# Optimization experiments

Hardware: AMD Instinct MI355X
Metric: run time of the kernel (lower is better)

The kernel has to match this reference:

```python
import jax, jax.numpy as jnp
import numpy as np

HEADS = 8  # from init_kwargs

def setup_inputs() -> dict:
    key = jax.random.key(0)
    ks = jax.random.split(key, 9)
    N, S, E = 8, 2048, 512
    scale = 1.0 / np.sqrt(E)
    return {
        "values": jax.random.normal(ks[0], (N, S, E), jnp.float32),
        "keys": jax.random.normal(ks[1], (N, S, E), jnp.float32),
        "query": jax.random.normal(ks[2], (N, S, E), jnp.float32),
        "mask": jnp.ones((N, 1, 1, S), jnp.int32),
        "Wv": jax.random.normal(ks[3], (E, E), jnp.float32) * scale,
        "Wk": jax.random.normal(ks[4], (E, E), jnp.float32) * scale,
        "Wq": jax.random.normal(ks[5], (E, E), jnp.float32) * scale,
        "Wo": jax.random.normal(ks[6], (E, E), jnp.float32) * scale,
        "bo": jnp.zeros((E,), jnp.float32),
    }

def reference(values, keys, query, mask, Wv, Wk, Wq, Wo, bo):
    N, Q, E = query.shape
    H = HEADS
    D = E // H
    v = (values @ Wv).reshape(N, -1, H, D)  # [N,K,H,D]
    k = (keys @ Wk).reshape(N, -1, H, D)
    q = (query @ Wq).reshape(N, Q, H, D)
    energy = jnp.einsum('nqhd,nkhd->nhqk', q, k)  # [N,H,Q,K]
    energy = jnp.where(mask == 0, jnp.float32(-1e20), energy)
    attn = jax.nn.softmax(energy / jnp.sqrt(jnp.float32(D)), axis=3)
    out = jnp.einsum('nhqk,nkhd->nqhd', attn, v).reshape(N, Q, E)
    return out @ Wo + bo
```

## Files before the change

kernel.cpp:

```cpp
#include <hip/hip_runtime.h>
#include <hip/hip_bf16.h>
#include <stdint.h>

typedef __bf16 bf16;
typedef __bf16 bf16x8 __attribute__((ext_vector_type(8)));
typedef __bf16 bf16x4v __attribute__((ext_vector_type(4)));
typedef float  f32x4  __attribute__((ext_vector_type(4)));
typedef float  f32x16 __attribute__((ext_vector_type(16)));
typedef unsigned int u32x4 __attribute__((ext_vector_type(4)));

#define NB    8
#define SEQ   2048
#define EMB   512
#define NHEAD 8
#define HD    64

static __device__ __forceinline__ f32x4 mfma16(bf16x8 a, bf16x8 b, f32x4 c) {
    return __builtin_amdgcn_mfma_f32_16x16x32_bf16(a, b, c, 0, 0, 0);
}
static __device__ __forceinline__ f32x16 mfma32(bf16x8 a, bf16x8 b, f32x16 c) {
    return __builtin_amdgcn_mfma_f32_32x32x16_bf16(a, b, c, 0, 0, 0);
}
static __device__ __forceinline__ float ex2(float x) {
    float r; asm("v_exp_f32 %0, %1" : "=v"(r) : "v"(x)); return r;
}
static __device__ __forceinline__ unsigned pkbf(float lo, float hi) {
    unsigned d; asm("v_cvt_pk_bf16_f32 %0, %1, %2" : "=v"(d) : "v"(lo), "v"(hi)); return d;
}
static __device__ __forceinline__ void gload_lds16(const void* g, void* l) {
    __builtin_amdgcn_global_load_lds(
        (const __attribute__((address_space(1))) unsigned int*)g,
        (__attribute__((address_space(3))) unsigned int*)l, 16, 0, 0);
}
#define PRIO1 __builtin_amdgcn_s_setprio(1)
#define PRIO0 __builtin_amdgcn_s_setprio(0)

__global__ __launch_bounds__(256) void prep_weights(
    const float* __restrict__ Wv, const float* __restrict__ Wk,
    const float* __restrict__ Wq, const float* __restrict__ Wo,
    bf16* __restrict__ wt)
{
    __shared__ float Ls[64][65];
    const int b    = blockIdx.x;
    const int wsel = b >> 6;
    const int kt   = (b & 63) >> 3;
    const int nt   = b & 7;
    const int t    = threadIdx.x;
    const float* src = (wsel == 0) ? Wv : (wsel == 1) ? Wk : (wsel == 2) ? Wq : Wo;

#pragma unroll
    for (int i = 0; i < 16; ++i) {
        int e = i * 256 + t;
        int k = e >> 6, n = e & 63;
        Ls[k][n] = src[(size_t)(kt * 64 + k) * 512 + nt * 64 + n];
    }
    __syncthreads();
#pragma unroll
    for (int i = 0; i < 16; ++i) {
        int e = i * 256 + t;
        int n = e >> 6, k = e & 63;
        wt[(size_t)wsel * 262144 + (size_t)(nt * 64 + n) * 512 + kt * 64 + k] = (bf16)Ls[k][n];
    }
}

template <bool A_F32, bool FINAL>
__global__ __launch_bounds__(256) void gemm_kernel(
    const void* __restrict__ Ap, const bf16* __restrict__ Bt,
    void* __restrict__ Cp, const float* __restrict__ bias, float oscale)
{
    __shared__ __align__(16) char AsM[128 * 144];
    __shared__ __align__(16) bf16 Bs[128][64];

    const int t    = threadIdx.x;
    const int lane = t & 63;
    const int wave = t >> 6;
    const int wr   = wave >> 1, wc = wave & 1;
    const int l15  = lane & 15, lg = lane >> 4;
    const long row0 = (long)blockIdx.x * 128;
    const int  col0 = blockIdx.y * 128;

    f32x4 acc[4][4];
#pragma unroll
    for (int i = 0; i < 4; i++)
#pragma unroll
        for (int j = 0; j < 4; j++) acc[i][j] = (f32x4){0.f, 0.f, 0.f, 0.f};

    for (int k0 = 0; k0 < 512; k0 += 64) {
        __syncthreads();
        if (A_F32) {
            const float* A = (const float*)Ap;
#pragma unroll
            for (int i = 0; i < 8; i++) {
                int c  = t + 256 * i;
                int r  = c >> 4;
                int cc = (c & 15) * 4;
                f32x4 v = *(const f32x4*)(A + (row0 + r) * 512 + k0 + cc);
                bf16x4v pk = { (bf16)v[0], (bf16)v[1], (bf16)v[2], (bf16)v[3] };
                *(bf16x4v*)(AsM + r * 144 + cc * 2) = pk;
            }
        } else {
            const bf16* A = (const bf16*)Ap;
#pragma unroll
            for (int i = 0; i < 4; i++) {
                int chunk = i * 4 + wave;
                int c = chunk * 64 + lane;
                int r = c >> 3, u = c & 7;
                gload_lds16(A + (row0 + r) * 512 + k0 + ((u ^ (r & 7)) << 3),
                            AsM + chunk * 1024);
            }
        }
#pragma unroll
        for (int i = 0; i < 4; i++) {
            int chunk = i * 4 + wave;
            int c = chunk * 64 + lane;
            int r = c >> 3, u = c & 7;
            gload_lds16(Bt + (size_t)(col0 + r) * 512 + k0 + ((u ^ (r & 7)) << 3),
                        (char*)&Bs[0][0] + chunk * 1024);
        }
        __syncthreads();
#pragma unroll
        for (int kc = 0; kc < 64; kc += 32) {
            bf16x8 af[4], bfv[4];
#pragma unroll
            for (int mb = 0; mb < 4; mb++) {
                int row = wr * 64 + mb * 16 + l15;
                if (A_F32)
                    af[mb] = *(bf16x8*)(AsM + row * 144 + (kc + lg * 8) * 2);
                else
                    af[mb] = *(bf16x8*)(AsM + row * 128 + (((lg + (kc >> 3)) ^ (l15 & 7)) << 4));
            }
#pragma unroll
            for (int nb = 0; nb < 4; nb++) {
                int row = wc * 64 + nb * 16 + l15;
                bfv[nb] = *(bf16x8*)((char*)&Bs[0][0] + row * 128 + (((lg + (kc >> 3)) ^ (l15 & 7)) << 4));
            }
#pragma unroll
            for (int mb = 0; mb < 4; mb++)
#pragma unroll
                for (int nb = 0; nb < 4; nb++)
                    acc[mb][nb] = mfma16(af[mb], bfv[nb], acc[mb][nb]);
        }
    }

#pragma unroll
    for (int mb = 0; mb < 4; mb++)
#pragma unroll
        for (int nb = 0; nb < 4; nb++)
#pragma unroll
            for (int r = 0; r < 4; r++) {
                long grow = row0 + wr * 64 + mb * 16 + lg * 4 + r;
                int  gcol = col0 + wc * 64 + nb * 16 + l15;
                float v = acc[mb][nb][r];
                if (FINAL) {
                    ((float*)Cp)[grow * 512 + gcol] = v + bias[gcol];
                } else {
                    ((bf16*)Cp)[grow * 512 + gcol] = (bf16)(v * oscale);
                }
            }
}

__global__ __launch_bounds__(512, 2) void attn_kernel(
    const bf16* __restrict__ Qg, const bf16* __restrict__ Kg,
    const bf16* __restrict__ Vg, const int* __restrict__ mask,
    bf16* __restrict__ ctx)
{
    __shared__ __align__(16) bf16 Ks[4][4096];
    __shared__ __align__(16) bf16 Vt[4][4096];
    __shared__ __align__(16) bf16 Ob[8][32 * 72];

    const int t    = threadIdx.x;
    const int lane = t & 63;
    const int w    = t >> 6;
    const int l31  = lane & 31;
    const int hi   = lane >> 5;
    const int h = blockIdx.x, n = blockIdx.y, qt = blockIdx.z;

    const size_t nbase   = (size_t)n * SEQ;
    const size_t headoff = (size_t)h * 64;
    const int q0 = qt * 512 + w * 64;

    const int k5_  = lane & 31;
    const int hi2_ = (k5_ >> 2) & 1;
    const int r_   = (k5_ & 3) + 4 * (k5_ >> 3);
    const int vpos = ((lane >> 5) * 2 + (r_ >> 3)) * 16 + hi2_ * 8 + (r_ & 7);

    int* mflags = (int*)&Ob[0][0];
    {
        const int* mp0 = mask + n * SEQ + t * 4;
        int mok = (mp0[0] != 0) & (mp0[1] != 0) & (mp0[2] != 0) & (mp0[3] != 0);
        unsigned long long b = __ballot(mok);
        if (lane == 0) mflags[w] = (b == ~0ULL) ? 1 : 0;
    }

    bf16x8 qf[2][4];
#pragma unroll
    for (int qb = 0; qb < 2; ++qb)
#pragma unroll
        for (int ds = 0; ds < 4; ++ds)
            qf[qb][ds] = *(const bf16x8*)(Qg + (nbase + q0 + qb * 32 + l31) * 512 + headoff + ds * 16 + hi * 8);

    f32x16 o[2][2] = {};
    float l_run[2] = {0.f, 0.f};

    const bf16* kg = Kg + (nbase + w * 8 + (lane >> 3)) * 512 + headoff + (((lane & 7) ^ (lane >> 3)) << 3);
    const bf16* vg = Vg + (nbase + lane) * 512 + headoff + w * 8;
    const int*  mp = mask + n * SEQ;

#define VSCAT(VR, VB) do {                                                    \
        char* vbp = (char*)(VB);                                              \
        _Pragma("unroll") for (int j = 0; j < 8; ++j)                         \
            *(bf16*)(vbp + (8 * w + j) * 128 + ((2 * vpos) ^ (j << 4))) = (VR)[j]; \
    } while (0)

    gload_lds16(kg,                     (char*)&Ks[0][0] + w * 1024);
    gload_lds16(kg + (size_t)64 * 512,  (char*)&Ks[1][0] + w * 1024);
    bf16x8 vrA = *(const bf16x8*)vg;
    bf16x8 vrB = *(const bf16x8*)(vg + (size_t)64 * 512);
    VSCAT(vrA, &Vt[0][0]);
    VSCAT(vrB, &Vt[1][0]);
    __syncthreads();
    const int maskall = mflags[0] & mflags[1] & mflags[2] & mflags[3] &
                        mflags[4] & mflags[5] & mflags[6] & mflags[7];

    f32x16 p[2][2];
    u32x4  bq[2][4];

#define QK_TILE(KB) do {                                                      \
        const char* kbb = (const char*)(KB);                                  \
        f32x16 zz = {};                                                       \
        p[0][0] = zz; p[0][1] = zz; p[1][0] = zz; p[1][1] = zz;               \
        PRIO1;                                                                \
        _Pragma("unroll")                                                     \
        for (int ds = 0; ds < 4; ++ds) {                                      \
            int sw = (ds * 32 + hi * 16) ^ ((l31 & 7) << 4);                  \
            bf16x8 kf0 = *(const bf16x8*)(kbb + l31 * 128 + sw);              \
            bf16x8 kf1 = *(const bf16x8*)(kbb + (32 + l31) * 128 + sw);       \
            p[0][0] = mfma32(kf0, qf[0][ds], p[0][0]);                        \
            p[1][0] = mfma32(kf0, qf[1][ds], p[1][0]);                        \
            p[0][1] = mfma32(kf1, qf[0][ds], p[0][1]);                        \
            p[1][1] = mfma32(kf1, qf[1][ds], p[1][1]);                        \
        }                                                                     \
        PRIO0;                                                                \
    } while (0)

#define MASK_TILE(T) do {                                                     \
        if (!maskall) {                                                       \
            int mv = mp[(T) * 64 + lane];                                     \
            unsigned long long mb = __ballot(mv != 0);                        \
            if (mb != ~0ULL) {                                                \
                _Pragma("unroll") for (int qb = 0; qb < 2; ++qb)              \
                _Pragma("unroll") for (int kb = 0; kb < 2; ++kb) {            \
                    float* pp = (float*)&p[qb][kb];                           \
                    _Pragma("unroll") for (int r = 0; r < 16; ++r) {          \
                        int kk = kb * 32 + (r & 3) + 8 * (r >> 2) + 4 * hi;   \
                        if (!((mb >> kk) & 1)) pp[r] = -1e30f;                \
                    }                                                         \
                }                                                             \
            }                                                                 \
        }                                                                     \
    } while (0)

#define SM_PACK do {                                                          \
        _Pragma("unroll")                                                     \
        for (int qb = 0; qb < 2; ++qb) {                                      \
            float* p0 = (float*)&p[qb][0];                                    \
            float* p1 = (float*)&p[qb][1];                                    \
            float sa0 = 0.f, sa1 = 0.f, sa2 = 0.f, sa3 = 0.f;                 \
            _Pragma("unroll") for (int r = 0; r < 16; r += 4) {               \
                float e0 = ex2(p0[r]);   p0[r]   = e0; sa0 += e0;             \
                float e1 = ex2(p0[r+1]); p0[r+1] = e1; sa1 += e1;             \
                float e2 = ex2(p0[r+2]); p0[r+2] = e2; sa2 += e2;             \
                float e3 = ex2(p0[r+3]); p0[r+3] = e3; sa3 += e3;             \
            }                                                                 \
            _Pragma("unroll") for (int r = 0; r < 16; r += 4) {               \
                float e0 = ex2(p1[r]);   p1[r]   = e0; sa0 += e0;             \
                float e1 = ex2(p1[r+1]); p1[r+1] = e1; sa1 += e1;             \
                float e2 = ex2(p1[r+2]); p1[r+2] = e2; sa2 += e2;             \
                float e3 = ex2(p1[r+3]); p1[r+3] = e3; sa3 += e3;             \
            }                                                                 \
            float sl = (sa0 + sa1) + (sa2 + sa3);                             \
            l_run[qb] += sl + __shfl_xor(sl, 32);                             \
            _Pragma("unroll")                                                 \
            for (int ks = 0; ks < 4; ++ks) {                                  \
                float* ps = (ks >> 1) ? p1 : p0;                              \
                int bo = (ks & 1) * 8;                                        \
                bq[qb][ks] = (u32x4){ pkbf(ps[bo + 0], ps[bo + 1]),           \
                                      pkbf(ps[bo + 2], ps[bo + 3]),           \
                                      pkbf(ps[bo + 4], ps[bo + 5]),           \
                                      pkbf(ps[bo + 6], ps[bo + 7]) };         \
            }                                                                 \
        }                                                                     \
    } while (0)

#define PV_TILE(VB) do {                                                      \
        const char* vbb = (const char*)(VB);                                  \
        PRIO1;                                                                \
        _Pragma("unroll")                                                     \
        for (int ks = 0; ks < 4; ++ks) {                                      \
            int sw = (ks * 32 + hi * 16) ^ ((l31 & 7) << 4);                  \
            bf16x8 vf0 = *(const bf16x8*)(vbb + l31 * 128 + sw);              \
            bf16x8 vf1 = *(const bf16x8*)(vbb + (32 + l31) * 128 + sw);       \
            union { u32x4 u; bf16x8 v; } c0, c1;                              \
            c0.u = bq[0][ks]; c1.u = bq[1][ks];                               \
            o[0][0] = mfma32(vf0, c0.v, o[0][0]);                             \
            o[0][1] = mfma32(vf0, c1.v, o[0][1]);                             \
            o[1][0] = mfma32(vf1, c0.v, o[1][0]);                             \
            o[1][1] = mfma32(vf1, c1.v, o[1][1]);                             \
        }                                                                     \
        PRIO0;                                                                \
    } while (0)

    for (int e = 0; e < 16; ++e) {
        const int bA = (e & 1) * 2, bB = bA + 1;
        const int nA = bA ^ 2,      nB = bB ^ 2;
        if (e < 15) {
            gload_lds16(kg + (size_t)(2 * e + 2) * 64 * 512, (char*)&Ks[nA][0] + w * 1024);
            gload_lds16(kg + (size_t)(2 * e + 3) * 64 * 512, (char*)&Ks[nB][0] + w * 1024);
            vrA = *(const bf16x8*)(vg + (size_t)(2 * e + 2) * 64 * 512);
            vrB = *(const bf16x8*)(vg + (size_t)(2 * e + 3) * 64 * 512);
        }
        QK_TILE(&Ks[bA][0]);
        MASK_TILE(2 * e);
        SM_PACK;
        PV_TILE(&Vt[bA][0]);
        QK_TILE(&Ks[bB][0]);
        MASK_TILE(2 * e + 1);
        SM_PACK;
        PV_TILE(&Vt[bB][0]);
        if (e < 15) {
            VSCAT(vrA, &Vt[nA][0]);
            VSCAT(vrB, &Vt[nB][0]);
        }
        __syncthreads();
    }

#pragma unroll
    for (int qb = 0; qb < 2; ++qb) {
        float inv = 1.f / l_run[qb];
        bf16* ob = &Ob[w][0];
#pragma unroll
        for (int db = 0; db < 2; ++db) {
            float* oo = (float*)&o[db][qb];
#pragma unroll
            for (int r = 0; r < 16; ++r) {
                int d = db * 32 + (r & 3) + 8 * (r >> 2) + 4 * hi;
                ob[l31 * 72 + d] = (bf16)(oo[r] * inv);
            }
        }
#pragma unroll
        for (int i = 0; i < 2; ++i)
#pragma unroll
            for (int half = 0; half < 2; ++half) {
                int ql = i * 16 + (lane >> 2);
                int d8 = (lane & 3) * 8 + half * 32;
                bf16x8 vv = *(const bf16x8*)(ob + ql * 72 + d8);
                *(bf16x8*)(ctx + (nbase + q0 + qb * 32 + ql) * 512 + headoff + d8) = vv;
            }
    }
#undef VSCAT
#undef QK_TILE
#undef MASK_TILE
#undef SM_PACK
#undef PV_TILE
}

extern "C" void kernel_launch(void* const* d_in, const int* in_sizes, int n_in,
                              void* d_out, int out_size, void* d_ws, size_t ws_size,
                              hipStream_t stream) {
    (void)in_sizes; (void)n_in; (void)out_size; (void)ws_size;
    const float* values = (const float*)d_in[0];
    const float* keys   = (const float*)d_in[1];
    const float* query  = (const float*)d_in[2];
    const int*   mask   = (const int*)d_in[3];
    const float* Wv = (const float*)d_in[4];
    const float* Wk = (const float*)d_in[5];
    const float* Wq = (const float*)d_in[6];
    const float* Wo = (const float*)d_in[7];
    const float* bo = (const float*)d_in[8];
    float* out = (float*)d_out;

    char* ws = (char*)d_ws;
    bf16* wt = (bf16*)(ws);
    bf16* Qb = (bf16*)(ws + ((size_t)2  << 20));
    bf16* Kb = (bf16*)(ws + ((size_t)18 << 20));
    bf16* Vb = (bf16*)(ws + ((size_t)34 << 20));
    bf16* Cb = (bf16*)(ws + ((size_t)50 << 20));

    const float SC = 0.18033688011f;

    prep_weights<<<256, 256, 0, stream>>>(Wv, Wk, Wq, Wo, wt);
    gemm_kernel<true, false><<<dim3(128, 4), 256, 0, stream>>>(values, wt,              Vb, nullptr, 1.0f);
    gemm_kernel<true, false><<<dim3(128, 4), 256, 0, stream>>>(keys,   wt + 262144,     Kb, nullptr, 1.0f);
    gemm_kernel<true, false><<<dim3(128, 4), 256, 0, stream>>>(query,  wt + 2 * 262144, Qb, nullptr, SC);
    attn_kernel<<<dim3(8, 8, 4), 512, 0, stream>>>(Qb, Kb, Vb, mask, Cb);
    gemm_kernel<false, true><<<dim3(128, 4), 256, 0, stream>>>(Cb, wt + 3 * 262144, out, bo, 1.0f);
}
```

Before: 162.3 us.

## Fuse QKV projections and pre-transpose V into attention-ready layout

Merges the three projection GEMM launches into one grid over a z dimension. The V projection now writes its output already transposed and permuted into the layout the attention kernel's PV MFMA expects. The attention kernel can then load V tiles straight into LDS with global_load_lds instead of doing register loads and scalar scatter writes each iteration, which takes VALU and LDS-store work out of the inner loop. The cost is a more complex V epilogue (an LDS transpose plus an index permutation) in the projection kernel.

```diff
diff --git a/kernel.cpp b/kernel.cpp
--- a/kernel.cpp
+++ b/kernel.cpp
@@ -31,6 +31,12 @@
     __builtin_amdgcn_global_load_lds(
         (const __attribute__((address_space(1))) unsigned int*)g,
         (__attribute__((address_space(3))) unsigned int*)l, 16, 0, 0);
+}
+static __device__ __forceinline__ int vposInv(int pos) {
+    int p4  = pos >> 4;
+    int r   = ((p4 & 1) << 3) | (pos & 7);
+    int hi2 = (pos >> 3) & 1;
+    return (p4 >> 1) * 32 + ((r & 3) | (hi2 << 2) | ((r >> 2) << 3));
 }
 #define PRIO1 __builtin_amdgcn_s_setprio(1)
 #define PRIO0 __builtin_amdgcn_s_setprio(0)
@@ -63,12 +69,122 @@
     }
 }
 
-template <bool A_F32, bool FINAL>
-__global__ __launch_bounds__(256) void gemm_kernel(
-    const void* __restrict__ Ap, const bf16* __restrict__ Bt,
-    void* __restrict__ Cp, const float* __restrict__ bias, float oscale)
+__global__ __launch_bounds__(256) void proj_fused(
+    const float* __restrict__ Av, const float* __restrict__ Ak,
+    const float* __restrict__ Aq, const bf16* __restrict__ wt,
+    bf16* __restrict__ VbP, bf16* __restrict__ Kb, bf16* __restrict__ Qb,
+    float sc)
 {
-    __shared__ __align__(16) char AsM[128 * 144];
+    __shared__ __align__(16) char smem[35328];
+    bf16* As = (bf16*)smem;
+    char* BsB = smem + 18432;
+
+    const int t    = threadIdx.x;
+    const int lane = t & 63;
+    const int wave = t >> 6;
+    const int wr   = wave >> 1, wc = wave & 1;
+    const int l15  = lane & 15, lg = lane >> 4;
+    const int z    = blockIdx.z;
+    const long row0 = (long)blockIdx.x * 128;
+    const int  col0 = blockIdx.y * 128;
+
+    const float* A  = (z == 0) ? Av : (z == 1) ? Ak : Aq;
+    const bf16*  Bt = wt + (size_t)z * 262144;
+    const float  oscale = (z == 2) ? sc : 1.0f;
+
+    f32x4 acc[4][4];
+#pragma unroll
+    for (int i = 0; i < 4; i++)
+#pragma unroll
+        for (int j = 0; j < 4; j++) acc[i][j] = (f32x4){0.f, 0.f, 0.f, 0.f};
+
+    for (int k0 = 0; k0 < 512; k0 += 64) {
+        __syncthreads();
+#pragma unroll
+        for (int i = 0; i < 8; i++) {
+            int c  = t + 256 * i;
+            int r  = c >> 4;
+            int cc = (c & 15) * 4;
+            f32x4 v = *(const f32x4*)(A + (row0 + r) * 512 + k0 + cc);
+            bf16x4v pk = { (bf16)v[0], (bf16)v[1], (bf16)v[2], (bf16)v[3] };
+            *(bf16x4v*)(As + r * 72 + cc) = pk;
+        }
+#pragma unroll
+        for (int i = 0; i < 4; i++) {
+            int chunk = i * 4 + wave;
+            int c = chunk * 64 + lane;
+            int r = c >> 3, u = c & 7;
+            gload_lds16(Bt + (size_t)(col0 + r) * 512 + k0 + ((u ^ (r & 7)) << 3),
+                        BsB + chunk * 1024);
+        }
+        __syncthreads();
+#pragma unroll
+        for (int kc = 0; kc < 64; kc += 32) {
+            bf16x8 af[4], bfv[4];
+#pragma unroll
+            for (int mb = 0; mb < 4; mb++)
+                af[mb] = *(bf16x8*)(As + (wr * 64 + mb * 16 + l15) * 72 + kc + lg * 8);
+#pragma unroll
+            for (int nb = 0; nb < 4; nb++) {
+                int row = wc * 64 + nb * 16 + l15;
+                bfv[nb] = *(bf16x8*)(BsB + row * 128 + (((lg + (kc >> 3)) ^ (l15 & 7)) << 4));
+            }
+#pragma unroll
+            for (int mb = 0; mb < 4; mb++)
+#pragma unroll
+                for (int nb = 0; nb < 4; nb++)
+                    acc[mb][nb] = mfma16(af[mb], bfv[nb], acc[mb][nb]);
+        }
+    }
+
+    if (z == 0) {
+        __syncthreads();
+        bf16* Cs = (bf16*)smem;
+#pragma unroll
+        for (int mb = 0; mb < 4; mb++)
+#pragma unroll
+            for (int nb = 0; nb < 4; nb++)
+#pragma unroll
+                for (int r = 0; r < 4; r++) {
+                    int keyl = wr * 64 + mb * 16 + lg * 4 + r;
+                    int dl   = wc * 64 + nb * 16 + l15;
+                    Cs[dl * 138 + keyl] = (bf16)acc[mb][nb][r];
+                }
+        __syncthreads();
+        const int n_idx = (int)(row0 >> 11);
+        const int key0  = (int)(row0 & 2047);
+        const int dl    = t >> 1;
+        const int half  = t & 1;
+        const int x8    = (dl & 7) << 3;
+        bf16* dst = VbP + ((size_t)n_idx * 512 + col0 + dl) * 2048 + key0 + half * 64;
+#pragma unroll
+        for (int cc = 0; cc < 8; ++cc) {
+            bf16x8 v;
+#pragma unroll
+            for (int j = 0; j < 8; ++j)
+                v[j] = Cs[dl * 138 + half * 64 + vposInv((cc * 8 + j) ^ x8)];
+            *(bf16x8*)(dst + cc * 8) = v;
+        }
+    } else {
+        bf16* Cp = (z == 1) ? Kb : Qb;
+#pragma unroll
+        for (int mb = 0; mb < 4; mb++)
+#pragma unroll
+            for (int nb = 0; nb < 4; nb++)
+#pragma unroll
+                for (int r = 0; r < 4; r++) {
+                    long grow = row0 + wr * 64 + mb * 16 + lg * 4 + r;
+                    int  gcol = col0 + wc * 64 + nb * 16 + l15;
+                    Cp[grow * 512 + gcol] = (bf16)(acc[mb][nb][r] * oscale);
+                }
+    }
+}
+
+__global__ __launch_bounds__(256) void gemm_final(
+    const bf16* __restrict__ Ap, const bf16* __restrict__ Bt,
+    float* __restrict__ Cp, const float* __restrict__ bias)
+{
+    __shared__ __align__(16) char AsM[128 * 128];
     __shared__ __align__(16) bf16 Bs[128][64];
 
     const int t    = threadIdx.x;
@@ -87,27 +203,13 @@
 
     for (int k0 = 0; k0 < 512; k0 += 64) {
         __syncthreads();
-        if (A_F32) {
-            const float* A = (const float*)Ap;
-#pragma unroll
-            for (int i = 0; i < 8; i++) {
-                int c  = t + 256 * i;
-                int r  = c >> 4;
-                int cc = (c & 15) * 4;
-                f32x4 v = *(const f32x4*)(A + (row0 + r) * 512 + k0 + cc);
-                bf16x4v pk = { (bf16)v[0], (bf16)v[1], (bf16)v[2], (bf16)v[3] };
-                *(bf16x4v*)(AsM + r * 144 + cc * 2) = pk;
-            }
-        } else {
-            const bf16* A = (const bf16*)Ap;
-#pragma unroll
-            for (int i = 0; i < 4; i++) {
-                int chunk = i * 4 + wave;
-                int c = chunk * 64 + lane;
-                int r = c >> 3, u = c & 7;
-                gload_lds16(A + (row0 + r) * 512 + k0 + ((u ^ (r & 7)) << 3),
-                            AsM + chunk * 1024);
-            }
+#pragma unroll
+        for (int i = 0; i < 4; i++) {
+            int chunk = i * 4 + wave;
+            int c = chunk * 64 + lane;
+            int r = c >> 3, u = c & 7;
+            gload_lds16(Ap + (row0 + r) * 512 + k0 + ((u ^ (r & 7)) << 3),
+                        AsM + chunk * 1024);
         }
 #pragma unroll
         for (int i = 0; i < 4; i++) {
@@ -124,10 +226,7 @@
 #pragma unroll
             for (int mb = 0; mb < 4; mb++) {
                 int row = wr * 64 + mb * 16 + l15;
-                if (A_F32)
-                    af[mb] = *(bf16x8*)(AsM + row * 144 + (kc + lg * 8) * 2);
-                else
-                    af[mb] = *(bf16x8*)(AsM + row * 128 + (((lg + (kc >> 3)) ^ (l15 & 7)) << 4));
+                af[mb] = *(bf16x8*)(AsM + row * 128 + (((lg + (kc >> 3)) ^ (l15 & 7)) << 4));
             }
 #pragma unroll
             for (int nb = 0; nb < 4; nb++) {
@@ -150,18 +249,13 @@
             for (int r = 0; r < 4; r++) {
                 long grow = row0 + wr * 64 + mb * 16 + lg * 4 + r;
                 int  gcol = col0 + wc * 64 + nb * 16 + l15;
-                float v = acc[mb][nb][r];
-                if (FINAL) {
-                    ((float*)Cp)[grow * 512 + gcol] = v + bias[gcol];
-                } else {
-                    ((bf16*)Cp)[grow * 512 + gcol] = (bf16)(v * oscale);
-                }
+                Cp[grow * 512 + gcol] = acc[mb][nb][r] + bias[gcol];
             }
 }
 
 __global__ __launch_bounds__(512, 2) void attn_kernel(
     const bf16* __restrict__ Qg, const bf16* __restrict__ Kg,
-    const bf16* __restrict__ Vg, const int* __restrict__ mask,
+    const bf16* __restrict__ VbP, const int* __restrict__ mask,
     bf16* __restrict__ ctx)
 {
     __shared__ __align__(16) bf16 Ks[4][4096];
@@ -179,11 +273,6 @@
     const size_t headoff = (size_t)h * 64;
     const int q0 = qt * 512 + w * 64;
 
-    const int k5_  = lane & 31;
-    const int hi2_ = (k5_ >> 2) & 1;
-    const int r_   = (k5_ & 3) + 4 * (k5_ >> 3);
-    const int vpos = ((lane >> 5) * 2 + (r_ >> 3)) * 16 + hi2_ * 8 + (r_ & 7);
-
     int* mflags = (int*)&Ob[0][0];
     {
         const int* mp0 = mask + n * SEQ + t * 4;
@@ -203,21 +292,13 @@
     float l_run[2] = {0.f, 0.f};
 
     const bf16* kg = Kg + (nbase + w * 8 + (lane >> 3)) * 512 + headoff + (((lane & 7) ^ (lane >> 3)) << 3);
-    const bf16* vg = Vg + (nbase + lane) * 512 + headoff + w * 8;
+    const bf16* vgP = VbP + ((size_t)n * 512 + h * 64 + w * 8 + (lane >> 3)) * 2048 + ((lane & 7) << 3);
     const int*  mp = mask + n * SEQ;
 
-#define VSCAT(VR, VB) do {                                                    \
-        char* vbp = (char*)(VB);                                              \
-        _Pragma("unroll") for (int j = 0; j < 8; ++j)                         \
-            *(bf16*)(vbp + (8 * w + j) * 128 + ((2 * vpos) ^ (j << 4))) = (VR)[j]; \
-    } while (0)
-
-    gload_lds16(kg,                     (char*)&Ks[0][0] + w * 1024);
-    gload_lds16(kg + (size_t)64 * 512,  (char*)&Ks[1][0] + w * 1024);
-    bf16x8 vrA = *(const bf16x8*)vg;
-    bf16x8 vrB = *(const bf16x8*)(vg + (size_t)64 * 512);
-    VSCAT(vrA, &Vt[0][0]);
-    VSCAT(vrB, &Vt[1][0]);
+    gload_lds16(kg,                    (char*)&Ks[0][0] + w * 1024);
+    gload_lds16(kg + (size_t)64 * 512, (char*)&Ks[1][0] + w * 1024);
+    gload_lds16(vgP,                   (char*)&Vt[0][0] + w * 1024);
+    gload_lds16(vgP + 64,              (char*)&Vt[1][0] + w * 1024);
     __syncthreads();
     const int maskall = mflags[0] & mflags[1] & mflags[2] & mflags[3] &
                         mflags[4] & mflags[5] & mflags[6] & mflags[7];
@@ -316,8 +397,8 @@
         if (e < 15) {
             gload_lds16(kg + (size_t)(2 * e + 2) * 64 * 512, (char*)&Ks[nA][0] + w * 1024);
             gload_lds16(kg + (size_t)(2 * e + 3) * 64 * 512, (char*)&Ks[nB][0] + w * 1024);
-            vrA = *(const bf16x8*)(vg + (size_t)(2 * e + 2) * 64 * 512);
-            vrB = *(const bf16x8*)(vg + (size_t)(2 * e + 3) * 64 * 512);
+            gload_lds16(vgP + (2 * e + 2) * 64,              (char*)&Vt[nA][0] + w * 1024);
+            gload_lds16(vgP + (2 * e + 3) * 64,              (char*)&Vt[nB][0] + w * 1024);
         }
         QK_TILE(&Ks[bA][0]);
         MASK_TILE(2 * e);
@@ -327,10 +408,6 @@
         MASK_TILE(2 * e + 1);
         SM_PACK;
         PV_TILE(&Vt[bB][0]);
-        if (e < 15) {
-            VSCAT(vrA, &Vt[nA][0]);
-            VSCAT(vrB, &Vt[nB][0]);
-        }
         __syncthreads();
     }
 
@@ -357,7 +434,6 @@
                 *(bf16x8*)(ctx + (nbase + q0 + qb * 32 + ql) * 512 + headoff + d8) = vv;
             }
     }
-#undef VSCAT
 #undef QK_TILE
 #undef MASK_TILE
 #undef SM_PACK
@@ -380,18 +456,17 @@
     float* out = (float*)d_out;
 
     char* ws = (char*)d_ws;
-    bf16* wt = (bf16*)(ws);
-    bf16* Qb = (bf16*)(ws + ((size_t)2  << 20));
-    bf16* Kb = (bf16*)(ws + ((size_t)18 << 20));
-    bf16* Vb = (bf16*)(ws + ((size_t)34 << 20));
-    bf16* Cb = (bf16*)(ws + ((size_t)50 << 20));
+    bf16* wt  = (bf16*)(ws);
+    bf16* Qb  = (bf16*)(ws + ((size_t)2  << 20));
+    bf16* Kb  = (bf16*)(ws + ((size_t)18 << 20));
+    bf16* VbP = (bf16*)(ws + ((size_t)34 << 20));
+    bf16* Cb  = (bf16*)(ws + ((size_t)50 << 20));
 
     const float SC = 0.18033688011f;
 
     prep_weights<<<256, 256, 0, stream>>>(Wv, Wk, Wq, Wo, wt);
-    gemm_kernel<true, false><<<dim3(128, 4), 256, 0, stream>>>(values, wt,              Vb, nullptr, 1.0f);
-    gemm_kernel<true, false><<<dim3(128, 4), 256, 0, stream>>>(keys,   wt + 262144,     Kb, nullptr, 1.0f);
-    gemm_kernel<true, false><<<dim3(128, 4), 256, 0, stream>>>(query,  wt + 2 * 262144, Qb, nullptr, SC);
-    attn_kernel<<<dim3(8, 8, 4), 512, 0, stream>>>(Qb, Kb, Vb, mask, Cb);
-    gemm_kernel<false, true><<<dim3(128, 4), 256, 0, stream>>>(Cb, wt + 3 * 262144, out, bo, 1.0f);
-}
+    proj_fused<<<dim3(128, 4, 3), 256, 0, stream>>>(values, keys, query, wt,
+                                                    VbP, Kb, Qb, SC);
+    attn_kernel<<<dim3(8, 8, 4), 512, 0, stream>>>(Qb, Kb, VbP, mask, Cb);
+    gemm_final<<<dim3(128, 4), 256, 0, stream>>>(Cb, wt + 3 * 262144, out, bo);
+}
```

Result: faster. 156.1 us (-3.8%).
